# Optimization experiments

Measured on AMD Instinct MI355X. Metric: run time of the kernel, lower is better.

The kernel has to match this reference:

```python
import jax, jax.numpy as jnp
import numpy as np

NUM_LAYERS = 4
D_MODEL = 512
D_INNER = 1024   # 2 * d_model (Mamba expand=2)
D_STATE = 16
DT_RANK = 32     # ceil(d_model / 16)
D_CONV = 4
BATCH = 2
SEQ = 512
EPS = 1e-5


def _rmsnorm(x, w, eps=EPS):
    # fused add+RMSNorm math: fp32 reduction, scale by weight (no bias)
    x = x.astype(jnp.float32)
    return x * jax.lax.rsqrt(jnp.mean(x * x, axis=-1, keepdims=True) + eps) * w


def _silu(x):
    return x * jax.nn.sigmoid(x)


def _causal_conv(x, w, b):
    # x: (B, D, L); w: (D, K) depthwise causal conv, left-pad K-1, take first L
    xp = jnp.pad(x, ((0, 0), (0, 0), (D_CONV - 1, 0)))
    out = jax.lax.conv_general_dilated(
        xp, w[:, None, :], (1,), 'VALID',
        dimension_numbers=('NCH', 'OIH', 'NCH'),
        feature_group_count=x.shape[1])
    return out + b[None, :, None]


def _selective_scan(u, delta, A, Bm, Cm):
    # u, delta: (B, D, L); A: (D, N); Bm, Cm: (B, N, L)
    xs = (jnp.moveaxis(delta, 2, 0), jnp.moveaxis(u, 2, 0),
          jnp.moveaxis(Bm, 2, 0), jnp.moveaxis(Cm, 2, 0))
    h0 = jnp.zeros((u.shape[0], u.shape[1], A.shape[1]), u.dtype)

    def step(h, xst):
        d_t, u_t, b_t, c_t = xst                     # (B,D),(B,D),(B,N),(B,N)
        dA = jnp.exp(d_t[:, :, None] * A[None])      # (B,D,N) ZOH discretization
        h = h * dA + (d_t * u_t)[:, :, None] * b_t[:, None, :]
        y = jnp.einsum('bdn,bn->bd', h, c_t)
        return h, y

    _, ys = jax.lax.scan(step, h0, xs)
    return jnp.moveaxis(ys, 0, 2)                    # (B, D, L)


def _ssm_branch(x, z, cw, cb, xpw, dtw, dtb, Alog, Dskip):
    x = _silu(_causal_conv(x, cw, cb))                              # (B, Din, L)
    x_dbl = jnp.einsum('rd,bdl->brl', xpw, x)                       # (B, R+2N, L)
    dt, Bm, Cm = jnp.split(x_dbl, [DT_RANK, DT_RANK + D_STATE], axis=1)
    delta = jax.nn.softplus(jnp.einsum('dr,brl->bdl', dtw, dt) + dtb[None, :, None])
    A = -jnp.exp(Alog.astype(jnp.float32))                          # (Din, N)
    y = _selective_scan(x, delta, A, Bm, Cm)
    y = y + Dskip[None, :, None] * x
    return y * _silu(z)


def _encoder(x, norm_w, in_proj_w, convw_f, convb_f, xpw_f, dtw_f, dtb_f,
             Alog_f, Dskip_f, convw_r, convb_r, xpw_r, dtw_r, dtb_r,
             Alog_r, Dskip_r, out_proj_w, normf_w):
    residual = None
    hs = x
    feats = []
    for i in range(NUM_LAYERS):
        # fused add + RMSNorm, prenorm=True, residual_in_fp32
        residual = hs if residual is None else (hs + residual)
        residual = residual.astype(jnp.float32)
        hn = _rmsnorm(residual, norm_w[i])
        # bimamba v2 mixer
        xz = jnp.einsum('ed,bld->bel', in_proj_w[i], hn)            # (B, 2Din, L)
        xi, zi = jnp.split(xz, 2, axis=1)
        y_f = _ssm_branch(xi, zi, convw_f[i], convb_f[i], xpw_f[i], dtw_f[i],
                          dtb_f[i], Alog_f[i], Dskip_f[i])
        y_r = _ssm_branch(xi[:, :, ::-1], zi[:, :, ::-1], convw_r[i], convb_r[i],
                          xpw_r[i], dtw_r[i], dtb_r[i], Alog_r[i], Dskip_r[i])
        y = y_f + y_r[:, :, ::-1]
        hs = jnp.einsum('bel,de->bld', y, out_proj_w[i])
        feats.append(hs)
    out = _rmsnorm(hs + residual, normf_w)                          # prenorm=False
    return out, feats


def setup_inputs() -> dict:
    key = jax.random.key(0)
    ks = jax.random.split(key, 12)
    Ly = NUM_LAYERS
    s = 0.02

    def nrm(k, shape):
        return jax.random.normal(k, shape, jnp.float32) * s

    dt = 1e-3 + jax.random.uniform(ks[11], (Ly, D_INNER), jnp.float32) * (0.1 - 1e-3)
    dtb = jnp.log(jnp.expm1(dt))  # inverse softplus of dt init
    Alog = jnp.log(jnp.broadcast_to(
        jnp.arange(1, D_STATE + 1, dtype=jnp.float32), (Ly, D_INNER, D_STATE)))
    return dict(
        x=jax.random.normal(ks[0], (BATCH, SEQ, D_MODEL), jnp.float32),
        norm_w=jnp.ones((Ly, D_MODEL), jnp.float32),
        in_proj_w=nrm(ks[1], (Ly, 2 * D_INNER, D_MODEL)),
        convw_f=nrm(ks[2], (Ly, D_INNER, D_CONV)),
        convb_f=jnp.zeros((Ly, D_INNER), jnp.float32),
        xpw_f=nrm(ks[3], (Ly, DT_RANK + 2 * D_STATE, D_INNER)),
        dtw_f=nrm(ks[4], (Ly, D_INNER, DT_RANK)),
        dtb_f=dtb,
        Alog_f=Alog,
        Dskip_f=jnp.ones((Ly, D_INNER), jnp.float32),
        convw_r=nrm(ks[5], (Ly, D_INNER, D_CONV)),
        convb_r=jnp.zeros((Ly, D_INNER), jnp.float32),
        xpw_r=nrm(ks[6], (Ly, DT_RANK + 2 * D_STATE, D_INNER)),
        dtw_r=nrm(ks[7], (Ly, D_INNER, DT_RANK)),
        dtb_r=dtb,
        Alog_r=Alog,
        Dskip_r=jnp.ones((Ly, D_INNER), jnp.float32),
        out_proj_w=nrm(ks[8], (Ly, D_MODEL, D_INNER)),
        normf_w=jnp.ones((D_MODEL,), jnp.float32),
    )


def reference(x, norm_w, in_proj_w, convw_f, convb_f, xpw_f, dtw_f, dtb_f,
              Alog_f, Dskip_f, convw_r, convb_r, xpw_r, dtw_r, dtb_r,
              Alog_r, Dskip_r, out_proj_w, normf_w):
    out, feats = _encoder(x, norm_w, in_proj_w, convw_f, convb_f, xpw_f, dtw_f,
                          dtb_f, Alog_f, Dskip_f, convw_r, convb_r, xpw_r,
                          dtw_r, dtb_r, Alog_r, Dskip_r, out_proj_w, normf_w)
    return (out, jnp.stack(feats))
```

## Files before the change

kernel.cpp:

```cpp
#include <hip/hip_runtime.h>

#define BATCH 2
#define SEQ 512
#define DMODEL 512
#define DINNER 1024
#define DSTATE 16
#define DTRANK 32
#define NBL (BATCH*SEQ)
#define EPSV 1e-5f

typedef __attribute__((ext_vector_type(8))) short bf16x8;
typedef __attribute__((ext_vector_type(4))) float f32x4;

static __device__ __forceinline__ float sigmoidf_(float x) {
  return 1.0f / (1.0f + __expf(-x));
}
static __device__ __forceinline__ float softplusf_(float x) {
  return fmaxf(x, 0.0f) + log1pf(__expf(-fabsf(x)));
}
static __device__ __forceinline__ unsigned short f2bf(float x) {
  unsigned int u = __float_as_uint(x);
  unsigned int r = (u + 0x7FFFu + ((u >> 16) & 1u)) >> 16;
  return (unsigned short)r;
}

__global__ __launch_bounds__(256) void wconvert_kernel(
    const float* __restrict__ s0, const float* __restrict__ s1,
    const float* __restrict__ s2, const float* __restrict__ s3,
    const float* __restrict__ s4, const float* __restrict__ s5,
    unsigned short* __restrict__ d0, unsigned short* __restrict__ d1,
    unsigned short* __restrict__ d2, unsigned short* __restrict__ d3,
    unsigned short* __restrict__ d4, unsigned short* __restrict__ d5) {
  long i = (long)(blockIdx.x * 256 + threadIdx.x) * 8;
  const float* src; unsigned short* dst;
  if (i < 4194304)      { src = s0; dst = d0; }
  else if (i < 6291456) { src = s1; dst = d1; i -= 4194304; }
  else if (i < 6553600) { src = s2; dst = d2; i -= 6291456; }
  else if (i < 6815744) { src = s3; dst = d3; i -= 6553600; }
  else if (i < 6946816) { src = s4; dst = d4; i -= 6815744; }
  else                  { src = s5; dst = d5; i -= 6946816; }
  const float4 v0 = *(const float4*)&src[i];
  const float4 v1 = *(const float4*)&src[i + 4];
  bf16x8 o;
  o[0] = (short)f2bf(v0.x); o[1] = (short)f2bf(v0.y);
  o[2] = (short)f2bf(v0.z); o[3] = (short)f2bf(v0.w);
  o[4] = (short)f2bf(v1.x); o[5] = (short)f2bf(v1.y);
  o[6] = (short)f2bf(v1.z); o[7] = (short)f2bf(v1.w);
  *(bf16x8*)&dst[i] = o;
}

__global__ __launch_bounds__(256) void addnorm_kernel(
    const float* __restrict__ hs, float* __restrict__ residual,
    const float* __restrict__ w, float* __restrict__ out,
    unsigned short* __restrict__ outb, int first) {
  const int row = blockIdx.x;
  const int t = threadIdx.x;
  const float* hp = hs + (long)row * DMODEL;
  float* rp = residual + (long)row * DMODEL;
  float r0 = hp[t], r1 = hp[t + 256];
  if (!first) { r0 += rp[t]; r1 += rp[t + 256]; }
  rp[t] = r0; rp[t + 256] = r1;
  float ss = r0 * r0 + r1 * r1;
  #pragma unroll
  for (int off = 32; off; off >>= 1) ss += __shfl_xor(ss, off, 64);
  __shared__ float sw[4];
  const int wid = t >> 6, lane = t & 63;
  if (lane == 0) sw[wid] = ss;
  __syncthreads();
  const float tot = sw[0] + sw[1] + sw[2] + sw[3];
  const float scale = rsqrtf(tot * (1.0f / (float)DMODEL) + EPSV);
  const float v0 = r0 * scale * w[t];
  const float v1 = r1 * scale * w[t + 256];
  if (out) {
    out[(long)row * DMODEL + t] = v0;
    out[(long)row * DMODEL + t + 256] = v1;
  }
  if (outb) {
    outb[(long)row * DMODEL + t] = f2bf(v0);
    outb[(long)row * DMODEL + t + 256] = f2bf(v1);
  }
}

#define LDK 40
#define LDK2 72

__global__ __launch_bounds__(256) void gemm_in_kernel(
    const unsigned short* __restrict__ A, const unsigned short* __restrict__ B,
    float* __restrict__ C) {
  __shared__ unsigned short As[128 * LDK2];
  __shared__ unsigned short Bs[64 * LDK2];
  const int t = threadIdx.x;
  const int m0 = blockIdx.y * 128, n0 = blockIdx.x * 64;
  const int lane = t & 63;
  const int w = t >> 6;
  const int wr = (w >> 1) * 64, wc = (w & 1) * 32;
  const int fr = lane & 15;
  const int fq = lane >> 4;
  const int K = DMODEL;

  f32x4 acc[4][2];
  #pragma unroll
  for (int i = 0; i < 4; ++i)
    #pragma unroll
    for (int j = 0; j < 2; ++j) {
      f32x4 z = {0.f, 0.f, 0.f, 0.f};
      acc[i][j] = z;
    }

  const int arow = t >> 1, ako = (t & 1) * 32;
  const int brow = t >> 2, bko = (t & 3) * 16;

  bf16x8 pa[4], pb[2];
  #define LOADG_IN(k0_) do {                                              \
    const unsigned short* ap = &A[(long)(m0 + arow) * K + (k0_) + ako];   \
    pa[0] = *(const bf16x8*)ap;        pa[1] = *(const bf16x8*)(ap + 8);  \
    pa[2] = *(const bf16x8*)(ap + 16); pa[3] = *(const bf16x8*)(ap + 24); \
    const unsigned short* bp = &B[(long)(n0 + brow) * K + (k0_) + bko];   \
// ... 55 lines not shown
  const int l0 = n0 & (SEQ - 1);
  const float* cw = dir ? cw_r : cw_f;
  const float* cb = dir ? cb_r : cb_f;
  float* xconv = dir ? xconv_r : xconv_f;
  unsigned short* dst = xcT + (long)dir * DINNER * NBL;
  const int t = threadIdx.x;
  const int c = t & 31, rr = t >> 5;
  #pragma unroll
  for (int p = 0; p < 4; ++p) {
    const int d = d0 + p * 8 + rr;
    const int l = l0 + c;
    const float* xi = xz + (long)d * NBL + b * SEQ;
    float sum = cb[d];
    #pragma unroll
    for (int k = 0; k < 4; ++k) {
      const int tt = l - 3 + k;
      if (tt >= 0) {
        const int src = dir ? (SEQ - 1 - tt) : tt;
        sum += cw[d * 4 + k] * xi[src];
      }
    }
    const float v = sum * sigmoidf_(sum);
    xconv[(long)d * NBL + n0 + c] = v;
    tile[p * 8 + rr][c] = f2bf(v);
  }
  __syncthreads();
  #pragma unroll
  for (int p = 0; p < 4; ++p) {
    const int n = n0 + p * 8 + rr;
    dst[(long)n * DINNER + d0 + c] = tile[c][p * 8 + rr];
  }
}

__global__ __launch_bounds__(256) void xdbl_mfma_kernel(
    const unsigned short* __restrict__ xpwb_f, const unsigned short* __restrict__ xpwb_r,
    const unsigned short* __restrict__ xcT,
    unsigned short* __restrict__ dtT,
    float* __restrict__ xbc_f, float* __restrict__ xbc_r) {
  __shared__ unsigned short As[64 * LDK2];
  __shared__ unsigned short Bs[128 * LDK2];
  const int t = threadIdx.x;
  const int dir = blockIdx.y;
  const int n0 = blockIdx.x * 128;
  const unsigned short* A = dir ? xpwb_r : xpwb_f;
  const unsigned short* B = xcT + (long)dir * DINNER * NBL;
  float* xbc = dir ? xbc_r : xbc_f;
  unsigned short* dtt = dtT + (long)dir * NBL * DTRANK;

  const int lane = t & 63;
  const int w = t >> 6;
  const int fr = lane & 15;
  const int fq = lane >> 4;

  f32x4 acc[4][2];
  #pragma unroll
  for (int i = 0; i < 4; ++i)
    #pragma unroll
    for (int j = 0; j < 2; ++j) {
      f32x4 z = {0.f, 0.f, 0.f, 0.f};
      acc[i][j] = z;
    }

  const int arow = t >> 2, ako = (t & 3) * 16;
  const int brow = t >> 1, bko = (t & 1) * 32;

  bf16x8 pa[2], pb[4];
  #define LOADG_XD(k0_) do {                                                   \
    const unsigned short* ap = &A[(long)arow * DINNER + (k0_) + ako];          \
    pa[0] = *(const bf16x8*)ap;        pa[1] = *(const bf16x8*)(ap + 8);       \
    const unsigned short* bp = &B[(long)(n0 + brow) * DINNER + (k0_) + bko];   \
    pb[0] = *(const bf16x8*)bp;        pb[1] = *(const bf16x8*)(bp + 8);       \
    pb[2] = *(const bf16x8*)(bp + 16); pb[3] = *(const bf16x8*)(bp + 24);      \
  } while (0)

  LOADG_XD(0);
  for (int k0 = 0; k0 < DINNER; k0 += 64) {
    if (k0) __syncthreads();
    *(bf16x8*)&As[arow * LDK2 + ako]      = pa[0];
    *(bf16x8*)&As[arow * LDK2 + ako + 8]  = pa[1];
    *(bf16x8*)&Bs[brow * LDK2 + bko]      = pb[0];
    *(bf16x8*)&Bs[brow * LDK2 + bko + 8]  = pb[1];
    *(bf16x8*)&Bs[brow * LDK2 + bko + 16] = pb[2];
    *(bf16x8*)&Bs[brow * LDK2 + bko + 24] = pb[3];
    __syncthreads();
    if (k0 + 64 < DINNER) LOADG_XD(k0 + 64);
    #pragma unroll
    for (int h = 0; h < 2; ++h) {
      bf16x8 af[4], bg[2];
      #pragma unroll
      for (int i = 0; i < 4; ++i)
        af[i] = *(const bf16x8*)&As[(i * 16 + fr) * LDK2 + h * 32 + fq * 8];
      #pragma unroll
      for (int j = 0; j < 2; ++j)
        bg[j] = *(const bf16x8*)&Bs[(w * 32 + j * 16 + fr) * LDK2 + h * 32 + fq * 8];
      #pragma unroll
      for (int i = 0; i < 4; ++i)
        #pragma unroll
        for (int j = 0; j < 2; ++j)
          acc[i][j] = __builtin_amdgcn_mfma_f32_16x16x32_bf16(
              af[i], bg[j], acc[i][j], 0, 0, 0);
    }
  }
  #undef LOADG_XD

  #pragma unroll
  for (int i = 0; i < 4; ++i)
    #pragma unroll
    for (int j = 0; j < 2; ++j)
      #pragma unroll
      for (int r2 = 0; r2 < 4; ++r2) {
        const int m = i * 16 + fq * 4 + r2;
        const int n = n0 + w * 32 + j * 16 + fr;
        const float v = acc[i][j][r2];
        if (m < DTRANK) dtt[(long)n * DTRANK + m] = f2bf(v);
        else xbc[(long)(m - 32) * NBL + n] = v;
      }
}

__global__ __launch_bounds__(256) void deltam_kernel(
    const unsigned short* __restrict__ dtwb_f, const unsigned short* __restrict__ dtwb_r,
    const unsigned short* __restrict__ dtT,
    const float* __restrict__ dtb_f, const float* __restrict__ dtb_r,
    float* __restrict__ delta_f, float* __restrict__ delta_r) {
  __shared__ unsigned short As[128 * LDK];
  __shared__ unsigned short Bs[128 * LDK];
  const int t = threadIdx.x;
  const int dir = blockIdx.z;
  const unsigned short* A = dir ? dtwb_r : dtwb_f;
  const unsigned short* B = dtT + (long)dir * NBL * DTRANK;
  const float* dtb = dir ? dtb_r : dtb_f;
  float* dl = dir ? delta_r : delta_f;
  const int m0 = blockIdx.y * 128, n0 = blockIdx.x * 128;
  const int lane = t & 63;
  const int w = t >> 6;
  const int wr = (w >> 1) * 64, wc = (w & 1) * 64;
  const int fr = lane & 15;
  const int fq = lane >> 4;

  const int srow = t >> 1;
  const int sko = (t & 1) * 16;
  *(bf16x8*)&As[srow * LDK + sko] =
      *(const bf16x8*)&A[(long)(m0 + srow) * DTRANK + sko];
  *(bf16x8*)&As[srow * LDK + sko + 8] =
      *(const bf16x8*)&A[(long)(m0 + srow) * DTRANK + sko + 8];
  *(bf16x8*)&Bs[srow * LDK + sko] =
      *(const bf16x8*)&B[(long)(n0 + srow) * DTRANK + sko];
  *(bf16x8*)&Bs[srow * LDK + sko + 8] =
      *(const bf16x8*)&B[(long)(n0 + srow) * DTRANK + sko + 8];
  __syncthreads();

  bf16x8 af[4], bg[4];
  #pragma unroll
  for (int i = 0; i < 4; ++i) {
    af[i] = *(const bf16x8*)&As[(wr + i * 16 + fr) * LDK + fq * 8];
    bg[i] = *(const bf16x8*)&Bs[(wc + i * 16 + fr) * LDK + fq * 8];
  }
  f32x4 acc[4][4];
  #pragma unroll
  for (int i = 0; i < 4; ++i)
    #pragma unroll
    for (int j = 0; j < 4; ++j) {
      f32x4 z = {0.f, 0.f, 0.f, 0.f};
      acc[i][j] = __builtin_amdgcn_mfma_f32_16x16x32_bf16(af[i], bg[j], z, 0, 0, 0);
    }

  #pragma unroll
  for (int i = 0; i < 4; ++i) {
    const int m = m0 + wr + i * 16 + fq * 4;
    #pragma unroll
    for (int r2 = 0; r2 < 4; ++r2) {
      const float bias = dtb[m + r2];
      #pragma unroll
      for (int j = 0; j < 4; ++j) {
        const int n = n0 + wc + j * 16 + fr;
        dl[(long)(m + r2) * NBL + n] = softplusf_(acc[i][j][r2] + bias);
      }
    }
  }
}

__global__ __launch_bounds__(256) void scan_wave_kernel(
    const float* __restrict__ delta_f, const float* __restrict__ delta_r,
    const float* __restrict__ xconv_f, const float* __restrict__ xconv_r,
    const float* __restrict__ xbc_f, const float* __restrict__ xbc_r,
    const float* __restrict__ Alog_f, const float* __restrict__ Alog_r,
    const float* __restrict__ Dsk_f, const float* __restrict__ Dsk_r,
    const float* __restrict__ xz,
    float* __restrict__ y_f, float* __restrict__ y_r) {
  const int t = threadIdx.x;
  const int wv = t >> 6;
  const int lane = t & 63;
  const int row = blockIdx.x * 4 + wv;
  const int dir = row >> 11, b = (row >> 10) & 1, d = row & 1023;

  const long rbase = (long)d * NBL + b * SEQ;
  const float* dp = (dir ? delta_r : delta_f) + rbase + lane * 8;
  const float* up = (dir ? xconv_r : xconv_f) + rbase + lane * 8;
  const float* bct = (dir ? xbc_r : xbc_f) + b * SEQ + lane * 8;
  const float* Alog = (dir ? Alog_r : Alog_f) + d * DSTATE;
  const float Dv = (dir ? Dsk_r : Dsk_f)[d];

  float dt[8], u[8], dtu[8], y[8];
  {
    const float4 a0 = *(const float4*)&dp[0];
    const float4 a1 = *(const float4*)&dp[4];
    dt[0] = a0.x; dt[1] = a0.y; dt[2] = a0.z; dt[3] = a0.w;
    dt[4] = a1.x; dt[5] = a1.y; dt[6] = a1.z; dt[7] = a1.w;
    const float4 b0 = *(const float4*)&up[0];
    const float4 b1 = *(const float4*)&up[4];
    u[0] = b0.x; u[1] = b0.y; u[2] = b0.z; u[3] = b0.w;
    u[4] = b1.x; u[5] = b1.y; u[6] = b1.z; u[7] = b1.w;
  }
  #pragma unroll
  for (int j = 0; j < 8; ++j) { dtu[j] = dt[j] * u[j]; y[j] = 0.f; }

  for (int n = 0; n < DSTATE; ++n) {
    const float An = -__expf(Alog[n]);
    float Bv[8], Cv[8], dA[8], cB[8];
    {
      const float* bp = bct + (long)n * NBL;
      const float* cp = bct + (long)(DSTATE + n) * NBL;
      const float4 b0 = *(const float4*)&bp[0];
      const float4 b1 = *(const float4*)&bp[4];
      Bv[0] = b0.x; Bv[1] = b0.y; Bv[2] = b0.z; Bv[3] = b0.w;
      Bv[4] = b1.x; Bv[5] = b1.y; Bv[6] = b1.z; Bv[7] = b1.w;
      const float4 c0 = *(const float4*)&cp[0];
      const float4 c1 = *(const float4*)&cp[4];
      Cv[0] = c0.x; Cv[1] = c0.y; Cv[2] = c0.z; Cv[3] = c0.w;
      Cv[4] = c1.x; Cv[5] = c1.y; Cv[6] = c1.z; Cv[7] = c1.w;
    }
    float h = 0.f, P = 1.f;
    #pragma unroll
    for (int j = 0; j < 8; ++j) {
      dA[j] = __expf(dt[j] * An);
      cB[j] = dtu[j] * Bv[j];
      h = fmaf(h, dA[j], cB[j]);
      P *= dA[j];
    }
    float hs = h, Ps = P;
    #pragma unroll
    for (int off = 1; off < 64; off <<= 1) {
      const float hp = __shfl_up(hs, off, 64);
      const float Pp = __shfl_up(Ps, off, 64);
      if (lane >= off) { hs = fmaf(hp, Ps, hs); Ps *= Pp; }
    }
    float h0 = __shfl_up(hs, 1, 64);
    if (lane == 0) h0 = 0.f;
    #pragma unroll
    for (int j = 0; j < 8; ++j) {
      h0 = fmaf(h0, dA[j], cB[j]);
      y[j] = fmaf(h0, Cv[j], y[j]);
    }
  }

  const float* zp = xz + (long)(DINNER + d) * NBL + b * SEQ;
  float* yp = (dir ? y_r : y_f) + rbase;
  #pragma unroll
  for (int j = 0; j < 8; ++j) {
    const int lg = lane * 8 + j;
    const int lo = dir ? (SEQ - 1 - lg) : lg;
    const float z = zp[lo];
    yp[lo] = fmaf(Dv, u[j], y[j]) * (z * sigmoidf_(z));
  }
}

__global__ __launch_bounds__(256) void ytrans_kernel(
    const float* __restrict__ yf, const float* __restrict__ yr,
    unsigned short* __restrict__ yt) {
  __shared__ unsigned short tile[32][33];
  const int e0 = blockIdx.y * 32, n0 = blockIdx.x * 32;
  const int t = threadIdx.x;
  const int c = t & 31, r8 = t >> 5;
  #pragma unroll
  for (int p = 0; p < 4; ++p) {
    const int e = e0 + p * 8 + r8;
    const float v = yf[(long)e * NBL + n0 + c] + yr[(long)e * NBL + n0 + c];
    tile[p * 8 + r8][c] = f2bf(v);
  }
  __syncthreads();
  #pragma unroll
  for (int p = 0; p < 4; ++p) {
    const int n = n0 + p * 8 + r8;
    yt[(long)n * DINNER + e0 + c] = tile[c][p * 8 + r8];
  }
}

__global__ __launch_bounds__(256) void gemm_out_kernel(
    const unsigned short* __restrict__ A, const unsigned short* __restrict__ B,
    float* __restrict__ C, float* __restrict__ C2) {
  __shared__ unsigned short As[128 * LDK2];
  __shared__ unsigned short Bs[128 * LDK2];
  const int t = threadIdx.x;
  const int m0 = blockIdx.y * 128, n0 = blockIdx.x * 128;
  const int lane = t & 63;
  const int w = t >> 6;
  const int wr = (w >> 1) * 64, wc = (w & 1) * 64;
  const int fr = lane & 15;
  const int fq = lane >> 4;
  const int K = DINNER;

  f32x4 acc[4][4];
  #pragma unroll
  for (int i = 0; i < 4; ++i)
    #pragma unroll
    for (int j = 0; j < 4; ++j) {
      f32x4 z = {0.f, 0.f, 0.f, 0.f};
      acc[i][j] = z;
    }

  const int srow = t >> 1, sko = (t & 1) * 32;

  bf16x8 pa[4], pb[4];
  #define LOADG_OUT(k0_) do {                                              \
    const unsigned short* ap = &A[(long)(m0 + srow) * K + (k0_) + sko];    \
    pa[0] = *(const bf16x8*)ap;        pa[1] = *(const bf16x8*)(ap + 8);   \
    pa[2] = *(const bf16x8*)(ap + 16); pa[3] = *(const bf16x8*)(ap + 24);  \
    const unsigned short* bp = &B[(long)(n0 + srow) * K + (k0_) + sko];    \
    pb[0] = *(const bf16x8*)bp;        pb[1] = *(const bf16x8*)(bp + 8);   \
    pb[2] = *(const bf16x8*)(bp + 16); pb[3] = *(const bf16x8*)(bp + 24);  \
  } while (0)

  LOADG_OUT(0);
// ... 5 lines not shown
    *(bf16x8*)&As[srow * LDK2 + sko + 24] = pa[3];
    *(bf16x8*)&Bs[srow * LDK2 + sko]      = pb[0];
    *(bf16x8*)&Bs[srow * LDK2 + sko + 8]  = pb[1];
    *(bf16x8*)&Bs[srow * LDK2 + sko + 16] = pb[2];
    *(bf16x8*)&Bs[srow * LDK2 + sko + 24] = pb[3];
    __syncthreads();
    if (k0 + 64 < K) LOADG_OUT(k0 + 64);
    #pragma unroll
    for (int h = 0; h < 2; ++h) {
      bf16x8 af[4], bg[4];
      #pragma unroll
      for (int i = 0; i < 4; ++i) {
        af[i] = *(const bf16x8*)&As[(wr + i * 16 + fr) * LDK2 + h * 32 + fq * 8];
        bg[i] = *(const bf16x8*)&Bs[(wc + i * 16 + fr) * LDK2 + h * 32 + fq * 8];
      }
      #pragma unroll
      for (int i = 0; i < 4; ++i)
        #pragma unroll
        for (int j = 0; j < 4; ++j)
          acc[i][j] = __builtin_amdgcn_mfma_f32_16x16x32_bf16(
              af[i], bg[j], acc[i][j], 0, 0, 0);
    }
  }
  #undef LOADG_OUT

  #pragma unroll
  for (int i = 0; i < 4; ++i)
    #pragma unroll
    for (int j = 0; j < 4; ++j)
      #pragma unroll
      for (int r2 = 0; r2 < 4; ++r2) {
        const int m = m0 + wr + i * 16 + fq * 4 + r2;
        const int n = n0 + wc + j * 16 + fr;
        const long addr = (long)n * DMODEL + m;
        C[addr] = acc[i][j][r2];
        C2[addr] = acc[i][j][r2];
      }
}

extern "C" void kernel_launch(void* const* d_in, const int* in_sizes, int n_in,
                              void* d_out, int out_size, void* d_ws, size_t ws_size,
                              hipStream_t stream) {
  (void)in_sizes; (void)n_in; (void)out_size; (void)ws_size;
  const float* x       = (const float*)d_in[0];
  const float* norm_w  = (const float*)d_in[1];
  const float* in_proj = (const float*)d_in[2];
  const float* convw_f = (const float*)d_in[3];
  const float* convb_f = (const float*)d_in[4];
  const float* xpw_f   = (const float*)d_in[5];
  const float* dtw_f   = (const float*)d_in[6];
  const float* dtb_f   = (const float*)d_in[7];
  const float* Alog_f  = (const float*)d_in[8];
  const float* Dsk_f   = (const float*)d_in[9];
  const float* convw_r = (const float*)d_in[10];
  const float* convb_r = (const float*)d_in[11];
  const float* xpw_r   = (const float*)d_in[12];
  const float* dtw_r   = (const float*)d_in[13];
  const float* dtb_r   = (const float*)d_in[14];
  const float* Alog_r  = (const float*)d_in[15];
  const float* Dsk_r   = (const float*)d_in[16];
  const float* out_w   = (const float*)d_in[17];
  const float* normf_w = (const float*)d_in[18];

  float* ws = (float*)d_ws;
  float* residual = ws;  ws += 524288;
  float* xzbuf    = ws;  ws += 2097152;
  float* xconv_f  = ws;  ws += 1048576;
  float* xconv_r  = ws;  ws += 1048576;
  float* xbc_f    = ws;  ws += 32768;
  float* xbc_r    = ws;  ws += 32768;
  float* delta_f  = ws;  ws += 1048576;
  float* delta_r  = ws;  ws += 1048576;
  float* y_f      = ws;  ws += 1048576;
  float* y_r      = ws;  ws += 1048576;
  float* hs       = ws;  ws += 524288;
  float* hnb_f    = ws;  ws += 262144;
  float* wbfin_f  = ws;  ws += 2097152;
  float* wbfout_f = ws;  ws += 1048576;
  float* ybt_f    = ws;  ws += 524288;
  float* xcT_f    = ws;  ws += 1048576;
  float* dtT_f    = ws;  ws += 32768;
  float* xpwb_f_  = ws;  ws += 131072;
  float* xpwb_r_  = ws;  ws += 131072;
  float* dtwb_f_  = ws;  ws += 65536;
  float* dtwb_r_  = ws;  ws += 65536;

  unsigned short* hnb = (unsigned short*)hnb_f;
  unsigned short* wbfin = (unsigned short*)wbfin_f;
  unsigned short* wbfout = (unsigned short*)wbfout_f;
  unsigned short* ybt = (unsigned short*)ybt_f;
  unsigned short* xcT = (unsigned short*)xcT_f;
  unsigned short* dtT = (unsigned short*)dtT_f;
  unsigned short* xpwb_f = (unsigned short*)xpwb_f_;
  unsigned short* xpwb_r = (unsigned short*)xpwb_r_;
  unsigned short* dtwb_f = (unsigned short*)dtwb_f_;
  unsigned short* dtwb_r = (unsigned short*)dtwb_r_;

  float* outp = (float*)d_out;

  wconvert_kernel<<<3456, 256, 0, stream>>>(
      in_proj, out_w, xpw_f, xpw_r, dtw_f, dtw_r,
      wbfin, wbfout, xpwb_f, xpwb_r, dtwb_f, dtwb_r);

  for (int layer = 0; layer < 4; ++layer) {
    addnorm_kernel<<<1024, 256, 0, stream>>>(
        layer == 0 ? x : hs, residual, norm_w + layer * DMODEL,
        nullptr, hnb, layer == 0 ? 1 : 0);
    gemm_in_kernel<<<dim3(16, 16), 256, 0, stream>>>(
        wbfin + (long)layer * 2048 * 512, hnb, xzbuf);
    conv_silu_kernel<<<dim3(32, 32, 2), 256, 0, stream>>>(
        xzbuf, convw_f + layer * DINNER * 4, convb_f + layer * DINNER,
        convw_r + layer * DINNER * 4, convb_r + layer * DINNER,
        xconv_f, xconv_r, xcT);
    xdbl_mfma_kernel<<<dim3(8, 2), 256, 0, stream>>>(
        xpwb_f + (long)layer * 64 * DINNER, xpwb_r + (long)layer * 64 * DINNER,
        xcT, dtT, xbc_f, xbc_r);
    deltam_kernel<<<dim3(8, 8, 2), 256, 0, stream>>>(
        dtwb_f + (long)layer * DINNER * DTRANK, dtwb_r + (long)layer * DINNER * DTRANK,
        dtT, dtb_f + layer * DINNER, dtb_r + layer * DINNER, delta_f, delta_r);
    scan_wave_kernel<<<1024, 256, 0, stream>>>(
        delta_f, delta_r, xconv_f, xconv_r, xbc_f, xbc_r,
        Alog_f + layer * DINNER * DSTATE, Alog_r + layer * DINNER * DSTATE,
        Dsk_f + layer * DINNER, Dsk_r + layer * DINNER,
        xzbuf, y_f, y_r);
    ytrans_kernel<<<dim3(32, 32), 256, 0, stream>>>(y_f, y_r, ybt);
    gemm_out_kernel<<<dim3(8, 4), 256, 0, stream>>>(
        wbfout + (long)layer * 512 * 1024, ybt, hs,
        outp + (long)(1 + layer) * 524288);
  }
  addnorm_kernel<<<1024, 256, 0, stream>>>(hs, residual, normf_w, outp, nullptr, 0);
}
```

Measured before the change: 392.5 us.

## Fold dt projection into precomputed combined weight and merge bidirectional scans

Precomputes dtw·xpw[:32] per layer and direction into a combined 1152×1024 weight, so a single fused GEMM over the conv output produces B/C and delta (with softplus) directly, replacing the separate x_dbl and delta GEMMs. The forward and reverse scans are merged into one kernel per (batch, channel) that adds the reversed-direction output via a lane shuffle, applies the z-gate, and writes a single y buffer. This removes a kernel launch, the dtT intermediate and one y buffer read in the transpose. In exchange the fused GEMM has K=1024 over 1152 rows (more FLOPs than the low-rank path), the composed weight is rounded to bf16, and each scan thread does twice the serial work.

```diff
diff --git a/kernel.cpp b/kernel.cpp
--- a/kernel.cpp
+++ b/kernel.cpp
@@ -49,6 +49,89 @@
   *(bf16x8*)&dst[i] = o;
 }
 
+__global__ __launch_bounds__(256) void prep_kernel(
+    const unsigned short* __restrict__ xpwb_f, const unsigned short* __restrict__ xpwb_r,
+    unsigned short* __restrict__ xpwT, unsigned short* __restrict__ Acomb) {
+  __shared__ unsigned short tile[32][33];
+  const int ld = blockIdx.y;
+  const int layer = ld >> 1, dir = ld & 1;
+  const unsigned short* xpwb = (dir ? xpwb_r : xpwb_f) + (long)layer * 64 * DINNER;
+  unsigned short* xT = xpwT + (long)ld * DINNER * DTRANK;
+  unsigned short* Ac = Acomb + (long)ld * 1152 * DINNER;
+  const int e0 = blockIdx.x * 32;
+  const int t = threadIdx.x;
+  const int c = t & 31, rr = t >> 5;
+  #pragma unroll
+  for (int p = 0; p < 4; ++p)
+    tile[p * 8 + rr][c] = xpwb[(long)(p * 8 + rr) * DINNER + e0 + c];
+  __syncthreads();
+  #pragma unroll
+  for (int p = 0; p < 4; ++p)
+    xT[(long)(e0 + p * 8 + rr) * DTRANK + c] = tile[c][p * 8 + rr];
+  #pragma unroll
+  for (int p = 0; p < 4; ++p)
+    Ac[(long)(p * 8 + rr) * DINNER + e0 + c] =
+        xpwb[(long)(32 + p * 8 + rr) * DINNER + e0 + c];
+  #pragma unroll
+  for (int q = 0; q < 3; ++q) {
+    unsigned short* zr = Ac + (long)(1056 + 3 * blockIdx.x + q) * DINNER;
+    ((unsigned long long*)zr)[t] = 0ULL;
+  }
+}
+
+#define LDK 40
+#define LDK2 72
+
+__global__ __launch_bounds__(256) void wdelta_kernel(
+    const unsigned short* __restrict__ dtwb_f, const unsigned short* __restrict__ dtwb_r,
+    const unsigned short* __restrict__ xpwT, unsigned short* __restrict__ Acomb) {
+  __shared__ unsigned short As[128 * LDK];
+  __shared__ unsigned short Bs[128 * LDK];
+  const int t = threadIdx.x;
+  const int ld = blockIdx.z;
+  const int layer = ld >> 1, dir = ld & 1;
+  const unsigned short* A = (dir ? dtwb_r : dtwb_f) + (long)layer * DINNER * DTRANK;
+  const unsigned short* B = xpwT + (long)ld * DINNER * DTRANK;
+  unsigned short* Ac = Acomb + (long)ld * 1152 * DINNER;
+  const int m0 = blockIdx.y * 128, n0 = blockIdx.x * 128;
+  const int lane = t & 63;
+  const int w = t >> 6;
+  const int wr = (w >> 1) * 64, wc = (w & 1) * 64;
+  const int fr = lane & 15;
+  const int fq = lane >> 4;
+
+  const int srow = t >> 1;
+  const int sko = (t & 1) * 16;
+  *(bf16x8*)&As[srow * LDK + sko] =
+      *(const bf16x8*)&A[(long)(m0 + srow) * DTRANK + sko];
+  *(bf16x8*)&As[srow * LDK + sko + 8] =
+      *(const bf16x8*)&A[(long)(m0 + srow) * DTRANK + sko + 8];
+  *(bf16x8*)&Bs[srow * LDK + sko] =
+      *(const bf16x8*)&B[(long)(n0 + srow) * DTRANK + sko];
+  *(bf16x8*)&Bs[srow * LDK + sko + 8] =
+      *(const bf16x8*)&B[(long)(n0 + srow) * DTRANK + sko + 8];
+  __syncthreads();
+
+  bf16x8 af[4], bg[4];
+  #pragma unroll
+  for (int i = 0; i < 4; ++i) {
+    af[i] = *(const bf16x8*)&As[(wr + i * 16 + fr) * LDK + fq * 8];
+    bg[i] = *(const bf16x8*)&Bs[(wc + i * 16 + fr) * LDK + fq * 8];
+  }
+  #pragma unroll
+  for (int i = 0; i < 4; ++i)
+    #pragma unroll
+    for (int j = 0; j < 4; ++j) {
+      f32x4 z = {0.f, 0.f, 0.f, 0.f};
+      const f32x4 a2 = __builtin_amdgcn_mfma_f32_16x16x32_bf16(af[i], bg[j], z, 0, 0, 0);
+      const int m = m0 + wr + i * 16 + fq * 4;
+      const int n = n0 + wc + j * 16 + fr;
+      #pragma unroll
+      for (int r2 = 0; r2 < 4; ++r2)
+        Ac[(long)(32 + m + r2) * DINNER + n] = f2bf(a2[r2]);
+    }
+}
+
 __global__ __launch_bounds__(256) void addnorm_kernel(
     const float* __restrict__ hs, float* __restrict__ residual,
     const float* __restrict__ w, float* __restrict__ out,
@@ -80,9 +163,6 @@
     outb[(long)row * DMODEL + t + 256] = f2bf(v1);
   }
 }
-
-#define LDK 40
-#define LDK2 72
 
 __global__ __launch_bounds__(256) void gemm_in_kernel(
     const unsigned short* __restrict__ A, const unsigned short* __restrict__ B,
@@ -204,103 +284,20 @@
   }
 }
 
-__global__ __launch_bounds__(256) void xdbl_mfma_kernel(
-    const unsigned short* __restrict__ xpwb_f, const unsigned short* __restrict__ xpwb_r,
-    const unsigned short* __restrict__ xcT,
-    unsigned short* __restrict__ dtT,
-    float* __restrict__ xbc_f, float* __restrict__ xbc_r) {
-  __shared__ unsigned short As[64 * LDK2];
+__global__ __launch_bounds__(256) void fusedproj_kernel(
+    const unsigned short* __restrict__ Acomb, const unsigned short* __restrict__ xcT,
+    const float* __restrict__ dtb_f, const float* __restrict__ dtb_r,
+    float* __restrict__ xbc_f, float* __restrict__ xbc_r,
+    float* __restrict__ delta_f, float* __restrict__ delta_r, int layer) {
+  __shared__ unsigned short As[128 * LDK2];
   __shared__ unsigned short Bs[128 * LDK2];
   const int t = threadIdx.x;
-  const int dir = blockIdx.y;
-  const int n0 = blockIdx.x * 128;
-  const unsigned short* A = dir ? xpwb_r : xpwb_f;
+  const int dir = blockIdx.z;
+  const int ld = layer * 2 + dir;
+  const unsigned short* A = Acomb + (long)ld * 1152 * DINNER;
   const unsigned short* B = xcT + (long)dir * DINNER * NBL;
+  const float* dtb = (dir ? dtb_r : dtb_f) + (long)layer * DINNER;
   float* xbc = dir ? xbc_r : xbc_f;
-  unsigned short* dtt = dtT + (long)dir * NBL * DTRANK;
-
-  const int lane = t & 63;
-  const int w = t >> 6;
-  const int fr = lane & 15;
-  const int fq = lane >> 4;
-
-  f32x4 acc[4][2];
-  #pragma unroll
-  for (int i = 0; i < 4; ++i)
-    #pragma unroll
-    for (int j = 0; j < 2; ++j) {
-      f32x4 z = {0.f, 0.f, 0.f, 0.f};
-      acc[i][j] = z;
-    }
-
-  const int arow = t >> 2, ako = (t & 3) * 16;
-  const int brow = t >> 1, bko = (t & 1) * 32;
-
-  bf16x8 pa[2], pb[4];
-  #define LOADG_XD(k0_) do {                                                   \
-    const unsigned short* ap = &A[(long)arow * DINNER + (k0_) + ako];          \
-    pa[0] = *(const bf16x8*)ap;        pa[1] = *(const bf16x8*)(ap + 8);       \
-    const unsigned short* bp = &B[(long)(n0 + brow) * DINNER + (k0_) + bko];   \
-    pb[0] = *(const bf16x8*)bp;        pb[1] = *(const bf16x8*)(bp + 8);       \
-    pb[2] = *(const bf16x8*)(bp + 16); pb[3] = *(const bf16x8*)(bp + 24);      \
-  } while (0)
-
-  LOADG_XD(0);
-  for (int k0 = 0; k0 < DINNER; k0 += 64) {
-    if (k0) __syncthreads();
-    *(bf16x8*)&As[arow * LDK2 + ako]      = pa[0];
-    *(bf16x8*)&As[arow * LDK2 + ako + 8]  = pa[1];
-    *(bf16x8*)&Bs[brow * LDK2 + bko]      = pb[0];
-    *(bf16x8*)&Bs[brow * LDK2 + bko + 8]  = pb[1];
-    *(bf16x8*)&Bs[brow * LDK2 + bko + 16] = pb[2];
-    *(bf16x8*)&Bs[brow * LDK2 + bko + 24] = pb[3];
-    __syncthreads();
-    if (k0 + 64 < DINNER) LOADG_XD(k0 + 64);
-    #pragma unroll
-    for (int h = 0; h < 2; ++h) {
-      bf16x8 af[4], bg[2];
-      #pragma unroll
-      for (int i = 0; i < 4; ++i)
-        af[i] = *(const bf16x8*)&As[(i * 16 + fr) * LDK2 + h * 32 + fq * 8];
-      #pragma unroll
-      for (int j = 0; j < 2; ++j)
-        bg[j] = *(const bf16x8*)&Bs[(w * 32 + j * 16 + fr) * LDK2 + h * 32 + fq * 8];
-      #pragma unroll
-      for (int i = 0; i < 4; ++i)
-        #pragma unroll
-        for (int j = 0; j < 2; ++j)
-          acc[i][j] = __builtin_amdgcn_mfma_f32_16x16x32_bf16(
-              af[i], bg[j], acc[i][j], 0, 0, 0);
-    }
-  }
-  #undef LOADG_XD
-
-  #pragma unroll
-  for (int i = 0; i < 4; ++i)
-    #pragma unroll
-    for (int j = 0; j < 2; ++j)
-      #pragma unroll
-      for (int r2 = 0; r2 < 4; ++r2) {
-        const int m = i * 16 + fq * 4 + r2;
-        const int n = n0 + w * 32 + j * 16 + fr;
-        const float v = acc[i][j][r2];
-        if (m < DTRANK) dtt[(long)n * DTRANK + m] = f2bf(v);
-        else xbc[(long)(m - 32) * NBL + n] = v;
-      }
-}
-
-__global__ __launch_bounds__(256) void deltam_kernel(
-    const unsigned short* __restrict__ dtwb_f, const unsigned short* __restrict__ dtwb_r,
-    const unsigned short* __restrict__ dtT,
-    const float* __restrict__ dtb_f, const float* __restrict__ dtb_r,
-    float* __restrict__ delta_f, float* __restrict__ delta_r) {
-  __shared__ unsigned short As[128 * LDK];
-  __shared__ unsigned short Bs[128 * LDK];
-  const int t = threadIdx.x;
-  const int dir = blockIdx.z;
-  const unsigned short* A = dir ? dtwb_r : dtwb_f;
-  const unsigned short* B = dtT + (long)dir * NBL * DTRANK;
-  const float* dtb = dir ? dtb_r : dtb_f;
   float* dl = dir ? delta_r : delta_f;
   const int m0 = blockIdx.y * 128, n0 = blockIdx.x * 128;
   const int lane = t & 63;
@@ -308,71 +305,83 @@
   const int wr = (w >> 1) * 64, wc = (w & 1) * 64;
   const int fr = lane & 15;
   const int fq = lane >> 4;
-
-  const int srow = t >> 1;
-  const int sko = (t & 1) * 16;
-  *(bf16x8*)&As[srow * LDK + sko] =
-      *(const bf16x8*)&A[(long)(m0 + srow) * DTRANK + sko];
-  *(bf16x8*)&As[srow * LDK + sko + 8] =
-      *(const bf16x8*)&A[(long)(m0 + srow) * DTRANK + sko + 8];
-  *(bf16x8*)&Bs[srow * LDK + sko] =
-      *(const bf16x8*)&B[(long)(n0 + srow) * DTRANK + sko];
-  *(bf16x8*)&Bs[srow * LDK + sko + 8] =
-      *(const bf16x8*)&B[(long)(n0 + srow) * DTRANK + sko + 8];
-  __syncthreads();
-
-  bf16x8 af[4], bg[4];
-  #pragma unroll
-  for (int i = 0; i < 4; ++i) {
-    af[i] = *(const bf16x8*)&As[(wr + i * 16 + fr) * LDK + fq * 8];
-    bg[i] = *(const bf16x8*)&Bs[(wc + i * 16 + fr) * LDK + fq * 8];
-  }
+  const int K = DINNER;
+
   f32x4 acc[4][4];
   #pragma unroll
   for (int i = 0; i < 4; ++i)
     #pragma unroll
     for (int j = 0; j < 4; ++j) {
       f32x4 z = {0.f, 0.f, 0.f, 0.f};
-      acc[i][j] = __builtin_amdgcn_mfma_f32_16x16x32_bf16(af[i], bg[j], z, 0, 0, 0);
-    }
-
-  #pragma unroll
-  for (int i = 0; i < 4; ++i) {
-    const int m = m0 + wr + i * 16 + fq * 4;
-    #pragma unroll
-    for (int r2 = 0; r2 < 4; ++r2) {
-      const float bias = dtb[m + r2];
-      #pragma unroll
-      for (int j = 0; j < 4; ++j) {
+      acc[i][j] = z;
+    }
+
+  const int srow = t >> 1, sko = (t & 1) * 32;
+
+  bf16x8 pa[4], pb[4];
+  #define LOADG_FP(k0_) do {                                               \
+    const unsigned short* ap = &A[(long)(m0 + srow) * K + (k0_) + sko];    \
+    pa[0] = *(const bf16x8*)ap;        pa[1] = *(const bf16x8*)(ap + 8);   \
+    pa[2] = *(const bf16x8*)(ap + 16); pa[3] = *(const bf16x8*)(ap + 24);  \
+    const unsigned short* bp = &B[(long)(n0 + srow) * K + (k0_) + sko];    \
+    pb[0] = *(const bf16x8*)bp;        pb[1] = *(const bf16x8*)(bp + 8);   \
+    pb[2] = *(const bf16x8*)(bp + 16); pb[3] = *(const bf16x8*)(bp + 24);  \
+  } while (0)
+
+  LOADG_FP(0);
+  for (int k0 = 0; k0 < K; k0 += 64) {
+    if (k0) __syncthreads();
+    *(bf16x8*)&As[srow * LDK2 + sko]      = pa[0];
+    *(bf16x8*)&As[srow * LDK2 + sko + 8]  = pa[1];
+    *(bf16x8*)&As[srow * LDK2 + sko + 16] = pa[2];
+    *(bf16x8*)&As[srow * LDK2 + sko + 24] = pa[3];
+    *(bf16x8*)&Bs[srow * LDK2 + sko]      = pb[0];
+    *(bf16x8*)&Bs[srow * LDK2 + sko + 8]  = pb[1];
+    *(bf16x8*)&Bs[srow * LDK2 + sko + 16] = pb[2];
+    *(bf16x8*)&Bs[srow * LDK2 + sko + 24] = pb[3];
+    __syncthreads();
+    if (k0 + 64 < K) LOADG_FP(k0 + 64);
+    #pragma unroll
+    for (int h = 0; h < 2; ++h) {
+      bf16x8 af[4], bg[4];
+      #pragma unroll
+      for (int i = 0; i < 4; ++i) {
+        af[i] = *(const bf16x8*)&As[(wr + i * 16 + fr) * LDK2 + h * 32 + fq * 8];
+        bg[i] = *(const bf16x8*)&Bs[(wc + i * 16 + fr) * LDK2 + h * 32 + fq * 8];
+      }
+      #pragma unroll
+      for (int i = 0; i < 4; ++i)
+        #pragma unroll
+        for (int j = 0; j < 4; ++j)
+          acc[i][j] = __builtin_amdgcn_mfma_f32_16x16x32_bf16(
+              af[i], bg[j], acc[i][j], 0, 0, 0);
+    }
+  }
+  #undef LOADG_FP
+
+  #pragma unroll
+  for (int i = 0; i < 4; ++i)
+    #pragma unroll
+    for (int j = 0; j < 4; ++j)
+      #pragma unroll
+      for (int r2 = 0; r2 < 4; ++r2) {
+        const int m = m0 + wr + i * 16 + fq * 4 + r2;
         const int n = n0 + wc + j * 16 + fr;
-        dl[(long)(m + r2) * NBL + n] = softplusf_(acc[i][j][r2] + bias);
+        const float v = acc[i][j][r2];
+        if (m < 32) {
+          xbc[(long)m * NBL + n] = v;
+        } else if (m < 1056) {
+          const int d = m - 32;
+          dl[(long)d * NBL + n] = softplusf_(v + dtb[d]);
+        }
       }
-    }
-  }
-}
-
-__global__ __launch_bounds__(256) void scan_wave_kernel(
-    const float* __restrict__ delta_f, const float* __restrict__ delta_r,
-    const float* __restrict__ xconv_f, const float* __restrict__ xconv_r,
-    const float* __restrict__ xbc_f, const float* __restrict__ xbc_r,
-    const float* __restrict__ Alog_f, const float* __restrict__ Alog_r,
-    const float* __restrict__ Dsk_f, const float* __restrict__ Dsk_r,
-    const float* __restrict__ xz,
-    float* __restrict__ y_f, float* __restrict__ y_r) {
-  const int t = threadIdx.x;
-  const int wv = t >> 6;
-  const int lane = t & 63;
-  const int row = blockIdx.x * 4 + wv;
-  const int dir = row >> 11, b = (row >> 10) & 1, d = row & 1023;
-
-  const long rbase = (long)d * NBL + b * SEQ;
-  const float* dp = (dir ? delta_r : delta_f) + rbase + lane * 8;
-  const float* up = (dir ? xconv_r : xconv_f) + rbase + lane * 8;
-  const float* bct = (dir ? xbc_r : xbc_f) + b * SEQ + lane * 8;
-  const float* Alog = (dir ? Alog_r : Alog_f) + d * DSTATE;
-  const float Dv = (dir ? Dsk_r : Dsk_f)[d];
-
-  float dt[8], u[8], dtu[8], y[8];
+}
+
+static __device__ __forceinline__ void scan_pass(
+    const float* __restrict__ dp, const float* __restrict__ up,
+    const float* __restrict__ bct, const float* __restrict__ Alog,
+    float Dv, int lane, float out[8], float u[8]) {
+  float dt[8], dtu[8];
   {
     const float4 a0 = *(const float4*)&dp[0];
     const float4 a1 = *(const float4*)&dp[4];
@@ -384,7 +393,7 @@
     u[4] = b1.x; u[5] = b1.y; u[6] = b1.z; u[7] = b1.w;
   }
   #pragma unroll
-  for (int j = 0; j < 8; ++j) { dtu[j] = dt[j] * u[j]; y[j] = 0.f; }
+  for (int j = 0; j < 8; ++j) { dtu[j] = dt[j] * u[j]; out[j] = 0.f; }
 
   for (int n = 0; n < DSTATE; ++n) {
     const float An = -__expf(Alog[n]);
@@ -421,24 +430,54 @@
     #pragma unroll
     for (int j = 0; j < 8; ++j) {
       h0 = fmaf(h0, dA[j], cB[j]);
-      y[j] = fmaf(h0, Cv[j], y[j]);
-    }
-  }
-
-  const float* zp = xz + (long)(DINNER + d) * NBL + b * SEQ;
-  float* yp = (dir ? y_r : y_f) + rbase;
+      out[j] = fmaf(h0, Cv[j], out[j]);
+    }
+  }
+  #pragma unroll
+  for (int j = 0; j < 8; ++j) out[j] = fmaf(Dv, u[j], out[j]);
+}
+
+__global__ __launch_bounds__(256) void scan_merged_kernel(
+    const float* __restrict__ delta_f, const float* __restrict__ delta_r,
+    const float* __restrict__ xconv_f, const float* __restrict__ xconv_r,
+    const float* __restrict__ xbc_f, const float* __restrict__ xbc_r,
+    const float* __restrict__ Alog_f, const float* __restrict__ Alog_r,
+    const float* __restrict__ Dsk_f, const float* __restrict__ Dsk_r,
+    const float* __restrict__ xz, float* __restrict__ y) {
+  const int t = threadIdx.x;
+  const int wv = t >> 6;
+  const int lane = t & 63;
+  const int row = blockIdx.x * 4 + wv;
+  const int b = row >> 10, d = row & 1023;
+  const long rbase = (long)d * NBL + b * SEQ;
+
+  float af[8], ar[8], uf[8], ur[8];
+  scan_pass(delta_f + rbase + lane * 8, xconv_f + rbase + lane * 8,
+            xbc_f + b * SEQ + lane * 8, Alog_f + d * DSTATE,
+            Dsk_f[d], lane, af, uf);
+  scan_pass(delta_r + rbase + lane * 8, xconv_r + rbase + lane * 8,
+            xbc_r + b * SEQ + lane * 8, Alog_r + d * DSTATE,
+            Dsk_r[d], lane, ar, ur);
+
+  const float* zp = xz + (long)(DINNER + d) * NBL + b * SEQ + lane * 8;
+  float* yp = y + rbase + lane * 8;
+  const float4 z0 = *(const float4*)&zp[0];
+  const float4 z1 = *(const float4*)&zp[4];
+  const float zv[8] = {z0.x, z0.y, z0.z, z0.w, z1.x, z1.y, z1.z, z1.w};
+  float out[8];
   #pragma unroll
   for (int j = 0; j < 8; ++j) {
-    const int lg = lane * 8 + j;
-    const int lo = dir ? (SEQ - 1 - lg) : lg;
-    const float z = zp[lo];
-    yp[lo] = fmaf(Dv, u[j], y[j]) * (z * sigmoidf_(z));
-  }
+    const float v = __shfl(ar[7 - j], 63 - lane, 64);
+    out[j] = (af[j] + v) * (zv[j] * sigmoidf_(zv[j]));
+  }
+  float4 o0 = {out[0], out[1], out[2], out[3]};
+  float4 o1 = {out[4], out[5], out[6], out[7]};
+  *(float4*)&yp[0] = o0;
+  *(float4*)&yp[4] = o1;
 }
 
 __global__ __launch_bounds__(256) void ytrans_kernel(
-    const float* __restrict__ yf, const float* __restrict__ yr,
-    unsigned short* __restrict__ yt) {
+    const float* __restrict__ yf, unsigned short* __restrict__ yt) {
   __shared__ unsigned short tile[32][33];
   const int e0 = blockIdx.y * 32, n0 = blockIdx.x * 32;
   const int t = threadIdx.x;
@@ -446,8 +485,7 @@
   #pragma unroll
   for (int p = 0; p < 4; ++p) {
     const int e = e0 + p * 8 + r8;
-    const float v = yf[(long)e * NBL + n0 + c] + yr[(long)e * NBL + n0 + c];
-    tile[p * 8 + r8][c] = f2bf(v);
+    tile[p * 8 + r8][c] = f2bf(yf[(long)e * NBL + n0 + c]);
   }
   __syncthreads();
   #pragma unroll
@@ -570,36 +608,39 @@
   float* xbc_r    = ws;  ws += 32768;
   float* delta_f  = ws;  ws += 1048576;
   float* delta_r  = ws;  ws += 1048576;
-  float* y_f      = ws;  ws += 1048576;
-  float* y_r      = ws;  ws += 1048576;
+  float* ybuf     = ws;  ws += 1048576;
   float* hs       = ws;  ws += 524288;
   float* hnb_f    = ws;  ws += 262144;
   float* wbfin_f  = ws;  ws += 2097152;
   float* wbfout_f = ws;  ws += 1048576;
   float* ybt_f    = ws;  ws += 524288;
   float* xcT_f    = ws;  ws += 1048576;
-  float* dtT_f    = ws;  ws += 32768;
   float* xpwb_f_  = ws;  ws += 131072;
   float* xpwb_r_  = ws;  ws += 131072;
   float* dtwb_f_  = ws;  ws += 65536;
   float* dtwb_r_  = ws;  ws += 65536;
+  float* xpwT_f   = ws;  ws += 131072;
+  float* Acomb_f  = ws;  ws += 4718592;
 
   unsigned short* hnb = (unsigned short*)hnb_f;
   unsigned short* wbfin = (unsigned short*)wbfin_f;
   unsigned short* wbfout = (unsigned short*)wbfout_f;
   unsigned short* ybt = (unsigned short*)ybt_f;
   unsigned short* xcT = (unsigned short*)xcT_f;
-  unsigned short* dtT = (unsigned short*)dtT_f;
   unsigned short* xpwb_f = (unsigned short*)xpwb_f_;
   unsigned short* xpwb_r = (unsigned short*)xpwb_r_;
   unsigned short* dtwb_f = (unsigned short*)dtwb_f_;
   unsigned short* dtwb_r = (unsigned short*)dtwb_r_;
+  unsigned short* xpwT = (unsigned short*)xpwT_f;
+  unsigned short* Acomb = (unsigned short*)Acomb_f;
 
   float* outp = (float*)d_out;
 
   wconvert_kernel<<<3456, 256, 0, stream>>>(
       in_proj, out_w, xpw_f, xpw_r, dtw_f, dtw_r,
       wbfin, wbfout, xpwb_f, xpwb_r, dtwb_f, dtwb_r);
+  prep_kernel<<<dim3(32, 8), 256, 0, stream>>>(xpwb_f, xpwb_r, xpwT, Acomb);
+  wdelta_kernel<<<dim3(8, 8, 8), 256, 0, stream>>>(dtwb_f, dtwb_r, xpwT, Acomb);
 
   for (int layer = 0; layer < 4; ++layer) {
     addnorm_kernel<<<1024, 256, 0, stream>>>(
@@ -611,18 +652,14 @@
         xzbuf, convw_f + layer * DINNER * 4, convb_f + layer * DINNER,
         convw_r + layer * DINNER * 4, convb_r + layer * DINNER,
         xconv_f, xconv_r, xcT);
-    xdbl_mfma_kernel<<<dim3(8, 2), 256, 0, stream>>>(
-        xpwb_f + (long)layer * 64 * DINNER, xpwb_r + (long)layer * 64 * DINNER,
-        xcT, dtT, xbc_f, xbc_r);
-    deltam_kernel<<<dim3(8, 8, 2), 256, 0, stream>>>(
-        dtwb_f + (long)layer * DINNER * DTRANK, dtwb_r + (long)layer * DINNER * DTRANK,
-        dtT, dtb_f + layer * DINNER, dtb_r + layer * DINNER, delta_f, delta_r);
-    scan_wave_kernel<<<1024, 256, 0, stream>>>(
+    fusedproj_kernel<<<dim3(8, 9, 2), 256, 0, stream>>>(
+        Acomb, xcT, dtb_f, dtb_r, xbc_f, xbc_r, delta_f, delta_r, layer);
+    scan_merged_kernel<<<512, 256, 0, stream>>>(
         delta_f, delta_r, xconv_f, xconv_r, xbc_f, xbc_r,
         Alog_f + layer * DINNER * DSTATE, Alog_r + layer * DINNER * DSTATE,
         Dsk_f + layer * DINNER, Dsk_r + layer * DINNER,
-        xzbuf, y_f, y_r);
-    ytrans_kernel<<<dim3(32, 32), 256, 0, stream>>>(y_f, y_r, ybt);
+        xzbuf, ybuf);
+    ytrans_kernel<<<dim3(32, 32), 256, 0, stream>>>(ybuf, ybt);
     gemm_out_kernel<<<dim3(8, 4), 256, 0, stream>>>(
         wbfout + (long)layer * 512 * 1024, ybt, hs,
         outp + (long)(1 + layer) * 524288);
```

After: 460.3 us. 17.3% more time.

## Merge forward and reverse scans in one wave and drop duplicate output writes

Applied to the files above, without the earlier changes.

The scan kernel now has each wave run both the forward and reverse selective scans for one (batch, channel) row. The two directions are combined in registers with a cross-lane shuffle that reverses the sequence order, then gated and written once with vectorized stores. This removes the separate y_r buffer and its extra read in the transpose kernel. The out-projection GEMM writes only to the output feature slice, which is then read back as the next layer's input, so the duplicate hs store goes away. The trade-off is half as many scan waves, each with twice the serial work, and higher register use per thread.

```diff
diff --git a/kernel.cpp b/kernel.cpp
--- a/kernel.cpp
+++ b/kernel.cpp
@@ -351,28 +351,11 @@
   }
 }
 
-__global__ __launch_bounds__(256) void scan_wave_kernel(
-    const float* __restrict__ delta_f, const float* __restrict__ delta_r,
-    const float* __restrict__ xconv_f, const float* __restrict__ xconv_r,
-    const float* __restrict__ xbc_f, const float* __restrict__ xbc_r,
-    const float* __restrict__ Alog_f, const float* __restrict__ Alog_r,
-    const float* __restrict__ Dsk_f, const float* __restrict__ Dsk_r,
-    const float* __restrict__ xz,
-    float* __restrict__ y_f, float* __restrict__ y_r) {
-  const int t = threadIdx.x;
-  const int wv = t >> 6;
-  const int lane = t & 63;
-  const int row = blockIdx.x * 4 + wv;
-  const int dir = row >> 11, b = (row >> 10) & 1, d = row & 1023;
-
-  const long rbase = (long)d * NBL + b * SEQ;
-  const float* dp = (dir ? delta_r : delta_f) + rbase + lane * 8;
-  const float* up = (dir ? xconv_r : xconv_f) + rbase + lane * 8;
-  const float* bct = (dir ? xbc_r : xbc_f) + b * SEQ + lane * 8;
-  const float* Alog = (dir ? Alog_r : Alog_f) + d * DSTATE;
-  const float Dv = (dir ? Dsk_r : Dsk_f)[d];
-
-  float dt[8], u[8], dtu[8], y[8];
+static __device__ __forceinline__ void scan_pass(
+    const float* __restrict__ dp, const float* __restrict__ up,
+    const float* __restrict__ bct, const float* __restrict__ Alog,
+    float Dv, int lane, float out[8], float u[8]) {
+  float dt[8], dtu[8];
   {
     const float4 a0 = *(const float4*)&dp[0];
     const float4 a1 = *(const float4*)&dp[4];
@@ -384,7 +367,7 @@
     u[4] = b1.x; u[5] = b1.y; u[6] = b1.z; u[7] = b1.w;
   }
   #pragma unroll
-  for (int j = 0; j < 8; ++j) { dtu[j] = dt[j] * u[j]; y[j] = 0.f; }
+  for (int j = 0; j < 8; ++j) { dtu[j] = dt[j] * u[j]; out[j] = 0.f; }
 
   for (int n = 0; n < DSTATE; ++n) {
     const float An = -__expf(Alog[n]);
@@ -421,24 +404,54 @@
     #pragma unroll
     for (int j = 0; j < 8; ++j) {
       h0 = fmaf(h0, dA[j], cB[j]);
-      y[j] = fmaf(h0, Cv[j], y[j]);
-    }
-  }
-
-  const float* zp = xz + (long)(DINNER + d) * NBL + b * SEQ;
-  float* yp = (dir ? y_r : y_f) + rbase;
+      out[j] = fmaf(h0, Cv[j], out[j]);
+    }
+  }
+  #pragma unroll
+  for (int j = 0; j < 8; ++j) out[j] = fmaf(Dv, u[j], out[j]);
+}
+
+__global__ __launch_bounds__(256) void scan_merged_kernel(
+    const float* __restrict__ delta_f, const float* __restrict__ delta_r,
+    const float* __restrict__ xconv_f, const float* __restrict__ xconv_r,
+    const float* __restrict__ xbc_f, const float* __restrict__ xbc_r,
+    const float* __restrict__ Alog_f, const float* __restrict__ Alog_r,
+    const float* __restrict__ Dsk_f, const float* __restrict__ Dsk_r,
+    const float* __restrict__ xz, float* __restrict__ y) {
+  const int t = threadIdx.x;
+  const int wv = t >> 6;
+  const int lane = t & 63;
+  const int row = blockIdx.x * 4 + wv;
+  const int b = row >> 10, d = row & 1023;
+  const long rbase = (long)d * NBL + b * SEQ;
+
+  float af[8], ar[8], uf[8], ur[8];
+  scan_pass(delta_f + rbase + lane * 8, xconv_f + rbase + lane * 8,
+            xbc_f + b * SEQ + lane * 8, Alog_f + d * DSTATE,
+            Dsk_f[d], lane, af, uf);
+  scan_pass(delta_r + rbase + lane * 8, xconv_r + rbase + lane * 8,
+            xbc_r + b * SEQ + lane * 8, Alog_r + d * DSTATE,
+            Dsk_r[d], lane, ar, ur);
+
+  const float* zp = xz + (long)(DINNER + d) * NBL + b * SEQ + lane * 8;
+  float* yp = y + rbase + lane * 8;
+  const float4 z0 = *(const float4*)&zp[0];
+  const float4 z1 = *(const float4*)&zp[4];
+  const float zv[8] = {z0.x, z0.y, z0.z, z0.w, z1.x, z1.y, z1.z, z1.w};
+  float out[8];
   #pragma unroll
   for (int j = 0; j < 8; ++j) {
-    const int lg = lane * 8 + j;
-    const int lo = dir ? (SEQ - 1 - lg) : lg;
-    const float z = zp[lo];
-    yp[lo] = fmaf(Dv, u[j], y[j]) * (z * sigmoidf_(z));
-  }
+    const float v = __shfl(ar[7 - j], 63 - lane, 64);
+    out[j] = (af[j] + v) * (zv[j] * sigmoidf_(zv[j]));
+  }
+  float4 o0 = {out[0], out[1], out[2], out[3]};
+  float4 o1 = {out[4], out[5], out[6], out[7]};
+  *(float4*)&yp[0] = o0;
+  *(float4*)&yp[4] = o1;
 }
 
 __global__ __launch_bounds__(256) void ytrans_kernel(
-    const float* __restrict__ yf, const float* __restrict__ yr,
-    unsigned short* __restrict__ yt) {
+    const float* __restrict__ yf, unsigned short* __restrict__ yt) {
   __shared__ unsigned short tile[32][33];
   const int e0 = blockIdx.y * 32, n0 = blockIdx.x * 32;
   const int t = threadIdx.x;
@@ -446,8 +459,7 @@
   #pragma unroll
   for (int p = 0; p < 4; ++p) {
     const int e = e0 + p * 8 + r8;
-    const float v = yf[(long)e * NBL + n0 + c] + yr[(long)e * NBL + n0 + c];
-    tile[p * 8 + r8][c] = f2bf(v);
+    tile[p * 8 + r8][c] = f2bf(yf[(long)e * NBL + n0 + c]);
   }
   __syncthreads();
   #pragma unroll
@@ -459,7 +471,7 @@
 
 __global__ __launch_bounds__(256) void gemm_out_kernel(
     const unsigned short* __restrict__ A, const unsigned short* __restrict__ B,
-    float* __restrict__ C, float* __restrict__ C2) {
+    float* __restrict__ C) {
   __shared__ unsigned short As[128 * LDK2];
   __shared__ unsigned short Bs[128 * LDK2];
   const int t = threadIdx.x;
@@ -531,9 +543,7 @@
       for (int r2 = 0; r2 < 4; ++r2) {
         const int m = m0 + wr + i * 16 + fq * 4 + r2;
         const int n = n0 + wc + j * 16 + fr;
-        const long addr = (long)n * DMODEL + m;
-        C[addr] = acc[i][j][r2];
-        C2[addr] = acc[i][j][r2];
+        C[(long)n * DMODEL + m] = acc[i][j][r2];
       }
 }
 
@@ -570,9 +580,7 @@
   float* xbc_r    = ws;  ws += 32768;
   float* delta_f  = ws;  ws += 1048576;
   float* delta_r  = ws;  ws += 1048576;
-  float* y_f      = ws;  ws += 1048576;
-  float* y_r      = ws;  ws += 1048576;
-  float* hs       = ws;  ws += 524288;
+  float* ybuf     = ws;  ws += 1048576;
   float* hnb_f    = ws;  ws += 262144;
   float* wbfin_f  = ws;  ws += 2097152;
   float* wbfout_f = ws;  ws += 1048576;
@@ -602,9 +610,9 @@
       wbfin, wbfout, xpwb_f, xpwb_r, dtwb_f, dtwb_r);
 
   for (int layer = 0; layer < 4; ++layer) {
+    const float* hsrc = layer == 0 ? x : (outp + (long)layer * 524288);
     addnorm_kernel<<<1024, 256, 0, stream>>>(
-        layer == 0 ? x : hs, residual, norm_w + layer * DMODEL,
-        nullptr, hnb, layer == 0 ? 1 : 0);
+        hsrc, residual, norm_w + layer * DMODEL, nullptr, hnb, layer == 0 ? 1 : 0);
     gemm_in_kernel<<<dim3(16, 16), 256, 0, stream>>>(
         wbfin + (long)layer * 2048 * 512, hnb, xzbuf);
     conv_silu_kernel<<<dim3(32, 32, 2), 256, 0, stream>>>(
@@ -617,15 +625,16 @@
     deltam_kernel<<<dim3(8, 8, 2), 256, 0, stream>>>(
         dtwb_f + (long)layer * DINNER * DTRANK, dtwb_r + (long)layer * DINNER * DTRANK,
         dtT, dtb_f + layer * DINNER, dtb_r + layer * DINNER, delta_f, delta_r);
-    scan_wave_kernel<<<1024, 256, 0, stream>>>(
+    scan_merged_kernel<<<512, 256, 0, stream>>>(
         delta_f, delta_r, xconv_f, xconv_r, xbc_f, xbc_r,
         Alog_f + layer * DINNER * DSTATE, Alog_r + layer * DINNER * DSTATE,
         Dsk_f + layer * DINNER, Dsk_r + layer * DINNER,
-        xzbuf, y_f, y_r);
-    ytrans_kernel<<<dim3(32, 32), 256, 0, stream>>>(y_f, y_r, ybt);
+        xzbuf, ybuf);
+    ytrans_kernel<<<dim3(32, 32), 256, 0, stream>>>(ybuf, ybt);
     gemm_out_kernel<<<dim3(8, 4), 256, 0, stream>>>(
-        wbfout + (long)layer * 512 * 1024, ybt, hs,
+        wbfout + (long)layer * 512 * 1024, ybt,
         outp + (long)(1 + layer) * 524288);
   }
-  addnorm_kernel<<<1024, 256, 0, stream>>>(hs, residual, normf_w, outp, nullptr, 0);
-}
+  addnorm_kernel<<<1024, 256, 0, stream>>>(
+      outp + 4 * 524288, residual, normf_w, outp, nullptr, 0);
+}
```

New measurement: 390.1 us. No clear change (-0.6%).
